# Performance work log

Measured on AMD Instinct MI355X. Metric: run time of the kernel, lower is better.

Reference implementation:

```python
import jax, jax.numpy as jnp
import numpy as np

N, H, DK, DV, DFF, D = 2, 8, 32, 32, 512, 256
B, S = 2, 2048
MASK_VALUE = -1e-30
EPS = 1e-14  # K.epsilon()**2 with default epsilon 1e-7


def glorot(key, shape):
    fan_in, fan_out = shape[-2], shape[-1]
    limit = np.sqrt(6.0 / (fan_in + fan_out))
    return jax.random.uniform(key, shape, jnp.float32, -limit, limit)


def setup_inputs() -> dict:
    key = jax.random.key(0)
    ks = jax.random.split(key, 8)
    return {
        "x": jax.random.normal(ks[0], (B, S, D), jnp.float32),
        "mask": jnp.ones((B, S), jnp.float32),
        "Wq": glorot(ks[1], (N, H, D, DK)),
        "Wk": glorot(ks[2], (N, H, D, DK)),
        "Wv": glorot(ks[3], (N, H, D, DV)),
        "Wo": glorot(ks[4], (N, H * DV, D)),
        "W1": glorot(ks[5], (N, D, DFF)),
        "b1": jnp.zeros((N, DFF), jnp.float32),
        "W2": glorot(ks[6], (N, DFF, D)),
        "b2": jnp.zeros((N, D), jnp.float32),
        "gamma": jnp.ones((2 * N,), jnp.float32),
        "beta": jnp.zeros((2 * N,), jnp.float32),
    }


def _layernorm(x, g, b):
    mean = jnp.mean(x, axis=-1, keepdims=True)
    var = jnp.mean(jnp.square(x - mean), axis=-1, keepdims=True)
    return (x - mean) / jnp.sqrt(var + EPS) * g + b


def reference(x, mask, Wq, Wk, Wv, Wo, W1, b1, W2, b2, gamma, beta):
    m = mask[:, None, None, :]  # [B,1,1,S], multiplies score rows' key axis
    for i in range(N):
        # batched multi-head attention (no 1/sqrt(dk) scaling, faithful to source)
        q = jnp.einsum("bsd,hdk->bhsk", x, Wq[i])
        k = jnp.einsum("bsd,hdk->bhsk", x, Wk[i])
        v = jnp.einsum("bsd,hdv->bhsv", x, Wv[i])
        A = jnp.einsum("bhsk,bhtk->bhst", q, k)  # [B,H,S,S]
        A = m * A + (1.0 - m) * MASK_VALUE
        A = jax.nn.softmax(A, axis=-1)
        o = jnp.einsum("bhst,bhtv->bhsv", A, v)
        conc = o.transpose(0, 2, 1, 3).reshape(x.shape[0], x.shape[1], H * DV)
        x = x + conc @ Wo[i]
        x = _layernorm(x, gamma[2 * i], beta[2 * i])
        ffn = jax.nn.relu(x @ W1[i] + b1[i]) @ W2[i] + b2[i]
        x = x + ffn
        x = _layernorm(x, gamma[2 * i + 1], beta[2 * i + 1])
    return x
```

## Files before the change

### kernel.cpp

```cpp
#include <hip/hip_runtime.h>
#include <hip/hip_bf16.h>

#define NL 2
#define NH 8
#define DKk 32
#define DVv 32
#define DFF 512
#define DD 256
#define BB 2
#define SS 2048
#define MROWS (BB*SS)
#define LN_EPS 1e-14f
#define L2E 1.4426950408889634f
#define SOFT_SHIFT_L2E (50.0f*L2E)

typedef __hip_bfloat16 bf16;
typedef unsigned short us;
typedef short bf16x8 __attribute__((ext_vector_type(8)));
typedef float f32x4  __attribute__((ext_vector_type(4)));
typedef unsigned short us4 __attribute__((ext_vector_type(4)));

#define O_XF   256
#define O_QB   (O_XF+1048576)
#define O_KH   (O_QB+1048576)
#define O_KL   (O_KH+524288)
#define O_VT   (O_KL+524288)
#define O_XH   (O_VT+524288)
#define O_XL   (O_XH+524288)
#define O_OP   (O_XL+524288)
#define O_ML   (O_OP+2097152)
#define O_MASK (O_ML+65536)
#define O_B1   (O_MASK+4096)
#define O_B2   (O_B1+1024)
#define O_GM   (O_B2+512)
#define O_BT   (O_GM+4)
#define O_PREP (O_BT+4)
#define TAIL_TOTAL (4096+1024+512+4+4)
#define CONV_BLOCKS (512 + (TAIL_TOTAL+255)/256)
#define PREP_BLOCKS 512
#define PQH 0u
#define PQL 393216u
#define POH 786432u
#define POL 917504u
#define P1H 1048576u
#define P1L 1310720u
#define P2H 1572864u
#define P2L 1835008u

__device__ __forceinline__ float us2f(us u){
  unsigned int v = ((unsigned int)u) << 16; float f;
  __builtin_memcpy(&f, &v, 4); return f;
}
__device__ __forceinline__ us f2bf_rne(float f){
  unsigned int b = __float_as_uint(f);
  b += 0x7FFFu + ((b>>16)&1u);
  return (us)(b>>16);
}

#if __has_builtin(__builtin_amdgcn_exp2f)
#define EXP2F(x) __builtin_amdgcn_exp2f(x)
#else
#define EXP2F(x) exp2f(x)
#endif

#if __has_builtin(__builtin_amdgcn_cvt_pk_bf16_f32)
typedef __bf16 bf16x2_t __attribute__((ext_vector_type(2)));
__device__ __forceinline__ int pack_bf16(float a, float b){
  bf16x2_t r = __builtin_amdgcn_cvt_pk_bf16_f32(a, b);
  int i; __builtin_memcpy(&i, &r, 4); return i;
}
#else
__device__ __forceinline__ int pack_bf16(float a, float b){
  int b0 = __float_as_int(a) + 0x8000;
  int b1 = __float_as_int(b) + 0x8000;
  return (b1 & 0xFFFF0000) | ((int)((unsigned)b0 >> 16));
}
#endif

__device__ __forceinline__ void gl_lds16(const us* g, us* l){
  __builtin_amdgcn_global_load_lds(
    (const __attribute__((address_space(1))) unsigned int*)g,
    (__attribute__((address_space(3))) unsigned int*)l, 16, 0, 0);
}

__device__ __forceinline__ size_t xhl_idx(int row, int col){
  int rt = row>>6, rg = (row>>4)&3, L15 = row&15;
  int kc = col>>5, Q = (col>>3)&3, j = col&7;
  return ((size_t)(rt*8+kc))*2048 + rg*512 + Q*128 + L15*8 + j;
}

__device__ __forceinline__ float conv1(const void* src, size_t i, int flag){
  if(flag) return ((const float*)src)[i];
  return us2f(((const us*)src)[i]);
}

__device__ __forceinline__ void prep_b_raw(const void* W0, const void* W1v, const void* W2v,
                                           int baseoff, us* __restrict__ Bh, us* __restrict__ Bl,
                                           int Kd, int Nd, int qkv, int g, int flag)
{
  int total = (Kd/32)*(Nd/16)*64;
  if(g >= total) return;
  int lane = g & 63, fi = g >> 6;
  int ncN = Nd/16;
  int nc = fi % ncN, kc = fi / ncN;
  int Q = lane>>4, L15 = lane&15;
  int n = nc*16 + L15;
  const void* src;
  int off0, stride;
  if(qkv){
    int sec = n>>8, h = (n>>5)&7, kq = n&31;
    src = (sec==0)?W0:((sec==1)?W1v:W2v);
    off0 = baseoff + h*8192 + kq;
    stride = 32;
  } else {
    src = W0;
    off0 = baseoff + n;
    stride = Nd;
  }
  #pragma unroll
  for(int j=0;j<8;j++){
    int k = kc*32 + Q*8 + j;
    float v = conv1(src, (size_t)off0 + (size_t)k*stride, flag);
    us hb = f2bf_rne(v);
    Bh[(size_t)g*8 + j] = hb;
    Bl[(size_t)g*8 + j] = f2bf_rne(v - us2f(hb));
  }
}

__global__ void conv_prep(const void* s0, const void* s1, const void* sWq, const void* sWk,
                          const void* sWv, const void* sWo, const void* sW1, const void* sb1,
                          const void* sW2, const void* sb2, const void* sgm, const void* sbt,
                          float* __restrict__ ws, int* __restrict__ flagp)
{
  __shared__ int fsh[4];
  int bad = 0;
  const us* xr = (const us*)s0;
  for(int i=threadIdx.x; i<4096; i+=256){
    float f = us2f(xr[i]);
    if(!(fabsf(f) < 1e3f)) bad = 1;
  }
  unsigned long long m = __ballot(bad);
  if((threadIdx.x&63)==0) fsh[threadIdx.x>>6] = (m!=0ull);
  __syncthreads();
  int flag = (fsh[0]|fsh[1]|fsh[2]|fsh[3]);
  if(blockIdx.x==0 && threadIdx.x==0) *flagp = flag;

  int b = blockIdx.x;
  if(b < PREP_BLOCKS){
    int layer = b >> 8, lb = b & 255;
    us* prep = (us*)(ws + O_PREP);
    if(lb < 96){
      int g = lb*256 + threadIdx.x;
      prep_b_raw(sWq, sWk, sWv, layer*65536, prep+PQH+(size_t)layer*196608,
                 prep+PQL+(size_t)layer*196608, 256, 768, 1, g, flag);
    } else if(lb < 128){
      int g = (lb-96)*256 + threadIdx.x;
      prep_b_raw(sWo, nullptr, nullptr, layer*65536, prep+POH+(size_t)layer*65536,
                 prep+POL+(size_t)layer*65536, 256, 256, 0, g, flag);
    } else if(lb < 192){
      int g = (lb-128)*256 + threadIdx.x;
      prep_b_raw(sW1, nullptr, nullptr, layer*131072, prep+P1H+(size_t)layer*131072,
                 prep+P1L+(size_t)layer*131072, 256, 512, 0, g, flag);
    } else {
      int g = (lb-192)*256 + threadIdx.x;
      prep_b_raw(sW2, nullptr, nullptr, layer*131072, prep+P2H+(size_t)layer*131072,
                 prep+P2L+(size_t)layer*131072, 512, 256, 0, g, flag);
    }
    return;
  }
  int b2 = b - PREP_BLOCKS;
  if(b2 < 512){
    int g8 = b2*256 + threadIdx.x;
    int e0 = g8*8;
    float v[8];
    if(flag){
      float4 a0 = *((const float4*)s0 + (e0>>2));
      float4 a1 = *((const float4*)s0 + (e0>>2) + 1);
      v[0]=a0.x; v[1]=a0.y; v[2]=a0.z; v[3]=a0.w;
      v[4]=a1.x; v[5]=a1.y; v[6]=a1.z; v[7]=a1.w;
    } else {
      bf16x8 u = *((const bf16x8*)s0 + g8);
      #pragma unroll
      for(int j=0;j<8;j++) v[j] = us2f((us)u[j]);
    }
    *(float4*)&ws[O_XF+e0]   = (float4){v[0],v[1],v[2],v[3]};
    *(float4*)&ws[O_XF+e0+4] = (float4){v[4],v[5],v[6],v[7]};
    union{ us a[8]; uint4 q; } hh, ll;
    #pragma unroll
    for(int j=0;j<8;j++){
      us hb = f2bf_rne(v[j]);
      hh.a[j] = hb;
      ll.a[j] = f2bf_rne(v[j] - us2f(hb));
    }
    size_t xi = xhl_idx(e0>>8, e0&255);
    *(uint4*)&((us*)(ws+O_XH))[xi] = hh.q;
    *(uint4*)&((us*)(ws+O_XL))[xi] = ll.q;
    return;
  }
  int g = (b2-512)*256 + threadIdx.x;
  if(g < 4096){ ws[O_MASK+g] = conv1(s1, g, flag)*L2E; return; }
  g -= 4096;
  if(g < 1024){ ws[O_B1+g] = conv1(sb1, g, flag); return; }
  g -= 1024;
  if(g < 512){ ws[O_B2+g] = conv1(sb2, g, flag); return; }
  g -= 512;
  if(g < 4){ ws[O_GM+g] = conv1(sgm, g, flag); return; }
  g -= 4;
  if(g < 4){ ws[O_BT+g] = conv1(sbt, g, flag); return; }
}

template<int MODE>
__launch_bounds__(256)
__global__ void gemm_mfma(const us* __restrict__ Axh, const us* __restrict__ Axl,
                          const us* __restrict__ Bh, const us* __restrict__ Bl,
                          const float* __restrict__ bias,
                          float* __restrict__ O,
                          us* __restrict__ QH, us* __restrict__ QL,
                          us* __restrict__ KH, us* __restrict__ KL, us* __restrict__ VT,
                          int Ncols, int Kdim)
{
  __shared__ __align__(16) us SH[16384];
  const int t = threadIdx.x;
  const int w = t>>6, lane = t&63;
  const int Q = lane>>4, L15 = lane&15;
  const int bx = blockIdx.x, by = blockIdx.y;
  const int row0 = bx*64;
  const int nc0 = by*4;
  const int col0 = by*64;
  const int nKc = Kdim>>5;
  const int ncW = Ncols>>4;

  f32x4 acc[2][2];
  #pragma unroll
  for(int i=0;i<2;i++)
    #pragma unroll
    for(int j=0;j<2;j++) acc[i][j] = (f32x4){0.f,0.f,0.f,0.f};

  auto stage = [&](int kc){
    const int bo = (kc&1)*8192;
    size_t abase = ((size_t)(bx*nKc + kc))*2048;
    gl_lds16(&Axh[abase + (size_t)t*8], &SH[bo + t*8]);
    gl_lds16(&Axl[abase + (size_t)t*8], &SH[bo + 2048 + t*8]);
    size_t gidx = ((size_t)(kc*ncW + nc0 + w)*64 + lane)*8;
    gl_lds16(&Bh[gidx], &SH[bo + 4096 + t*8]);
    gl_lds16(&Bl[gidx], &SH[bo + 6144 + t*8]);
  };

  stage(0);

  for(int kc=0; kc<nKc; kc++){
    __syncthreads();
    if(kc+1 < nKc) stage(kc+1);
    const int bo = (kc&1)*8192;
    const us* Ah  = SH + bo;
    const us* Al  = SH + bo + 2048;
    const us* Bhs = SH + bo + 4096;
    const us* Bls = SH + bo + 6144;

    bf16x8 aAh[2], aAl[2], bBh[2], bBl[2];
    #pragma unroll
    for(int rg2=0;rg2<2;rg2++){
      int rg = (w&1)*2 + rg2;
      aAh[rg2] = *(const bf16x8*)&Ah[rg*512 + lane*8];
      aAl[rg2] = *(const bf16x8*)&Al[rg*512 + lane*8];
    }
    #pragma unroll
    for(int cg2=0;cg2<2;cg2++){
      int nc = (w>>1)*2 + cg2;
      bBh[cg2] = *(const bf16x8*)&Bhs[nc*512 + lane*8];
      bBl[cg2] = *(const bf16x8*)&Bls[nc*512 + lane*8];
    }
    #pragma unroll
    for(int rg2=0;rg2<2;rg2++)
      #pragma unroll
      for(int cg2=0;cg2<2;cg2++){
        acc[rg2][cg2] = __builtin_amdgcn_mfma_f32_16x16x32_bf16(aAl[rg2], bBh[cg2], acc[rg2][cg2], 0,0,0);
        acc[rg2][cg2] = __builtin_amdgcn_mfma_f32_16x16x32_bf16(aAh[rg2], bBl[cg2], acc[rg2][cg2], 0,0,0);
        acc[rg2][cg2] = __builtin_amdgcn_mfma_f32_16x16x32_bf16(aAh[rg2], bBh[cg2], acc[rg2][cg2], 0,0,0);
      }
  }

  if(MODE==0){
    __syncthreads();
    us* TH = SH;
    us* TL = SH + 4608;
    #pragma unroll
    for(int rg2=0;rg2<2;rg2++)
      #pragma unroll
      for(int cg2=0;cg2<2;cg2++)
        #pragma unroll
        for(int r=0;r<4;r++){
          int rl = (w&1)*32 + rg2*16 + Q*4 + r;
          int cl = (w>>1)*32 + cg2*16 + L15;
          float va = acc[rg2][cg2][r];
          us hb = f2bf_rne(va);
          TH[rl*72+cl] = hb;
          TL[rl*72+cl] = f2bf_rne(va - us2f(hb));
        }
    __syncthreads();
    const int sec = col0>>8;
    const int h0  = (col0&255)>>5;
    const int b_  = row0>>11;
    const int srow0 = row0 & 2047;
    if(sec < 2){
      us* DH = (sec==0) ? QH : KH;
      us* DL = (sec==0) ? QL : KL;
      #pragma unroll
      for(int u2=0; u2<2; u2++){
        int u = w + u2*4;
        int rg = u&3, half = u>>2;
        int lbase = (rg*16 + L15)*72 + half*32 + Q*8;
        bf16x8 hv = *(const bf16x8*)&TH[lbase];
        bf16x8 lv = *(const bf16x8*)&TL[lbase];
        int bh = b_*NH + h0 + half;
        size_t dbase = ((size_t)(bh*128 + (srow0>>4) + rg)*64 + lane)*8;
        *(bf16x8*)&DH[dbase] = hv;
        *(bf16x8*)&DL[dbase] = lv;
      }
    } else {
      #pragma unroll
      for(int u2=0; u2<2; u2++){
        int u = w + u2*4;
        int sgrp = u&1, kqh = (u>>1)&1, half = u>>2;
        union{ us u8[8]; bf16x8 v; } vv;
        #pragma unroll
        for(int j=0;j<8;j++){
          int rl = sgrp*32 + Q*8 + j;
          int cl = half*32 + kqh*16 + L15;
          vv.u8[j] = TH[rl*72+cl];
        }
        int bh = b_*NH + h0 + half;
        size_t dbase = ((size_t)((bh*64 + (srow0>>5) + sgrp)*2 + kqh)*64 + lane)*8;
        *(bf16x8*)&VT[dbase] = vv.v;
      }
    }
  } else {
    #pragma unroll
    for(int rg2=0;rg2<2;rg2++)
      #pragma unroll
      for(int cg2=0;cg2<2;cg2++)
        #pragma unroll
        for(int r=0;r<4;r++){
          int row = row0 + (w&1)*32 + rg2*16 + Q*4 + r;
          int c   = col0 + (w>>1)*32 + cg2*16 + L15;
          float v = acc[rg2][cg2][r] + bias[c];
          O[(size_t)row*Ncols + c] = v>0.f ? v : 0.f;
        }
  }
}

template<int SRC>
__launch_bounds__(256)
__global__ void gemm_ln(const float* __restrict__ A,
                        const float* __restrict__ OpartA, const float* __restrict__ MLA,
                        const us* __restrict__ Bh, const us* __restrict__ Bl,
                        const float* __restrict__ bias, const float* __restrict__ res,
                        float* __restrict__ xf,
                        us* __restrict__ xh, us* __restrict__ xl,
                        const float* __restrict__ gamma, const float* __restrict__ beta, int gi,
                        void* __restrict__ out, int write_out,
                        const int* __restrict__ flagp, int Kdim)
{
  __shared__ __align__(16) us Ahs[1024], Als[1024];
  __shared__ __align__(16) us Bhs[16384], Bls[16384];
  __shared__ float lred[128];
  const int t = threadIdx.x;
  const int w = t>>6, lane = t&63;
  const int Q = lane>>4, L15 = lane&15;
  const int row0 = blockIdx.x*16;
  const int nKc = Kdim>>5;

  f32x4 acc[4];
  #pragma unroll
  for(int cg=0;cg<4;cg++) acc[cg] = (f32x4){0.f,0.f,0.f,0.f};

  float4 pv0, pv1, pv;
  float pl0 = 0.f, pl1 = 0.f;

  auto preloadA = [&](int kc){
    if(t < 128){
      int r = t>>3;
      int kl = (t&7)*4;
      if(SRC==0){
        int row = row0 + r;
        int b_ = row>>11, s_ = row&2047;
        size_t i0 = (size_t)(b_*8 + kc)*2048 + s_;
        pl0 = MLA[i0];
        pl1 = MLA[i0+32768];
        pv0 = *(const float4*)&OpartA[i0*32 + kl];
        pv1 = *(const float4*)&OpartA[(i0+32768)*32 + kl];
      } else {
        pv = *(const float4*)&A[(size_t)(row0+r)*Kdim + kc*32 + kl];
      }
    }
  };
  auto writeA = [&](int kc){
    if(t < 128){
      int r = t>>3;
      int kl = (t&7)*4;
      float f[4];
      if(SRC==0){
        float inv = 1.f/(pl0 + pl1);
        f[0]=(pv0.x+pv1.x)*inv; f[1]=(pv0.y+pv1.y)*inv;
        f[2]=(pv0.z+pv1.z)*inv; f[3]=(pv0.w+pv1.w)*inv;
      } else {
        f[0]=pv.x; f[1]=pv.y; f[2]=pv.z; f[3]=pv.w;
      }
      us4 h4, l4;
      #pragma unroll
      for(int j=0;j<4;j++){
        us hb = f2bf_rne(f[j]);
        h4[j] = hb; l4[j] = f2bf_rne(f[j] - us2f(hb));
      }
      int bo = (kc&1)*512;
      int off = (kl>>3)*128 + r*8 + (kl&7);
      *(us4*)&Ahs[bo+off] = h4;
      *(us4*)&Als[bo+off] = l4;
    }
  };
  auto stageB = [&](int kc){
    const int bo = (kc&1)*8192;
    #pragma unroll
    for(int ii=0; ii<4; ii++){
      int unit = w + ii*4;
      size_t gidx = ((size_t)(kc*16 + unit)*64 + lane)*8;
      gl_lds16(&Bh[gidx], &Bhs[bo + unit*512 + lane*8]);
      gl_lds16(&Bl[gidx], &Bls[bo + unit*512 + lane*8]);
    }
  };

  preloadA(0);
  stageB(0);
  writeA(0);

  for(int kc=0; kc<nKc; kc++){
    __syncthreads();
    if(kc+1 < nKc){
      preloadA(kc+1);
      stageB(kc+1);
    }
    const int bo = (kc&1);
    bf16x8 aAh = *(const bf16x8*)&Ahs[bo*512 + lane*8];
    bf16x8 aAl = *(const bf16x8*)&Als[bo*512 + lane*8];
    #pragma unroll
    for(int cg=0;cg<4;cg++){
      int unit = w*4 + cg;
      bf16x8 bBh = *(const bf16x8*)&Bhs[bo*8192 + unit*512 + lane*8];
      bf16x8 bBl = *(const bf16x8*)&Bls[bo*8192 + unit*512 + lane*8];
      acc[cg] = __builtin_amdgcn_mfma_f32_16x16x32_bf16(aAl, bBh, acc[cg], 0,0,0);
      acc[cg] = __builtin_amdgcn_mfma_f32_16x16x32_bf16(aAh, bBl, acc[cg], 0,0,0);
      acc[cg] = __builtin_amdgcn_mfma_f32_16x16x32_bf16(aAh, bBh, acc[cg], 0,0,0);
    }
    if(kc+1 < nKc) writeA(kc+1);
  }

  float tmp[4][4];
  #pragma unroll
  for(int cg=0;cg<4;cg++)
    #pragma unroll
    for(int r=0;r<4;r++){
      int row = row0 + Q*4 + r;
      int c = w*64 + cg*16 + L15;
      float v = acc[cg][r] + res[(size_t)row*DD + c];
      if(SRC==1) v += bias[c];
      tmp[cg][r] = v;
    }
  float s[4], sq[4];
  #pragma unroll
  for(int r=0;r<4;r++){
    s[r]  = tmp[0][r]+tmp[1][r]+tmp[2][r]+tmp[3][r];
    sq[r] = tmp[0][r]*tmp[0][r]+tmp[1][r]*tmp[1][r]+tmp[2][r]*tmp[2][r]+tmp[3][r]*tmp[3][r];
  }
  #pragma unroll
  for(int off=1; off<16; off<<=1)
    #pragma unroll
    for(int r=0;r<4;r++){
      s[r]  += __shfl_xor(s[r], off);
      sq[r] += __shfl_xor(sq[r], off);
    }
  if(L15==0){
    #pragma unroll
    for(int r=0;r<4;r++){
      int rl = Q*4 + r;
      lred[(w*16 + rl)*2]   = s[r];
      lred[(w*16 + rl)*2+1] = sq[r];
    }
  }
  __syncthreads();
  float g = gamma[gi], bb = beta[gi];
  float scv[4], mnv[4];
  #pragma unroll
  for(int r=0;r<4;r++){
    int rl = Q*4 + r;
    float S  = lred[rl*2]   + lred[(16+rl)*2]   + lred[(32+rl)*2]   + lred[(48+rl)*2];
    float SQ = lred[rl*2+1] + lred[(16+rl)*2+1] + lred[(32+rl)*2+1] + lred[(48+rl)*2+1];
    float mean = S*(1.f/DD);
    float var  = SQ*(1.f/DD) - mean*mean;
    scv[r] = rsqrtf(var+LN_EPS)*g;
    mnv[r] = mean;
  }
  int flag = write_out ? *flagp : 0;
  #pragma unroll
  for(int cg=0;cg<4;cg++)
    #pragma unroll
    for(int r=0;r<4;r++){
      int row = row0 + Q*4 + r;
      int c = w*64 + cg*16 + L15;
      float val = (tmp[cg][r]-mnv[r])*scv[r] + bb;
      xf[(size_t)row*DD + c] = val;
      us hb = f2bf_rne(val);
      size_t xi = xhl_idx(row, c);
      xh[xi] = hb;
      xl[xi] = f2bf_rne(val - us2f(hb));
      if(write_out){
        if(flag) ((float*)out)[(size_t)row*DD + c] = val;
        else     ((bf16*)out)[(size_t)row*DD + c] = __float2bfloat16(val);
      }
    }
}

__launch_bounds__(256)
__global__ void attn_kernel(const us* __restrict__ QH, const us* __restrict__ QL,
                            const us* __restrict__ KH, const us* __restrict__ KL,
                            const us* __restrict__ VT,
                            const float* __restrict__ mask,
                            float* __restrict__ Opart, float* __restrict__ ML)
{
  __shared__ __align__(16) us Khs[4096], Kls[4096], Vts[4096];
  __shared__ __align__(16) float Msl[1024];
  const int t = threadIdx.x;
  const int swz = (blockIdx.x & 7)*128 + (blockIdx.x >> 3);
  const int bh = swz >> 6;
  const int qt = (swz & 63) >> 1;
  const int ks = swz & 1;
  const int b_ = bh >> 3;
  const int wv = t >> 6;
  const int lane = t & 63;
  const int Q = lane >> 4, L15 = lane & 15;
  const int q0 = qt*64 + wv*16;

  size_t qidx = ((size_t)(bh*128 + qt*4 + wv)*64 + lane)*8;
  const bf16x8 qh_v = *(const bf16x8*)&QH[qidx];
  const bf16x8 ql_v = *(const bf16x8*)&QL[qidx];

  const us* KHbh = KH + (size_t)bh*65536;
  const us* KLbh = KL + (size_t)bh*65536;
  const us* VTbh = VT + (size_t)bh*65536;
  const int base = ks*1024;

  f32x4 Oa0a = {0.f,0.f,0.f,0.f}, Oa0b = {0.f,0.f,0.f,0.f};
  f32x4 Oa1a = {0.f,0.f,0.f,0.f}, Oa1b = {0.f,0.f,0.f,0.f};
  float lacc = 0.f;

  {
    const us* mrow = (const us*)(mask + (size_t)b_*SS + base);
    gl_lds16(mrow + (size_t)t*8, ((us*)Msl) + t*8);
    size_t kbase = (size_t)(base>>4)*512;
    size_t vbase = (size_t)(base>>5)*1024;
    gl_lds16(&KHbh[kbase + (size_t)t*8], &Khs[t*8]);
    gl_lds16(&KLbh[kbase + (size_t)t*8], &Kls[t*8]);
    gl_lds16(&VTbh[vbase + (size_t)t*8], &Vts[t*8]);
  }

  for(int s=0; s<16; s++){
    __syncthreads();
    if(s < 15){
      int t0n = base + (s+1)*64;
      int bn = (s+1)&1;
      size_t kbase = (size_t)(t0n>>4)*512;
      size_t vbase = (size_t)(t0n>>5)*1024;
      gl_lds16(&KHbh[kbase + (size_t)t*8], &Khs[bn*2048 + t*8]);
      gl_lds16(&KLbh[kbase + (size_t)t*8], &Kls[bn*2048 + t*8]);
      gl_lds16(&VTbh[vbase + (size_t)t*8], &Vts[bn*2048 + t*8]);
    }
    const int bo = (s&1)*2048;
    const int mo = s*64;

    f32x4 St[4];
    const f32x4 zz = {0.f,0.f,0.f,0.f};
    #pragma unroll
    for(int kt=0;kt<4;kt++){
      bf16x8 aKh = *(const bf16x8*)&Khs[bo + kt*512 + lane*8];
      bf16x8 aKl = *(const bf16x8*)&Kls[bo + kt*512 + lane*8];
      f32x4 a = __builtin_amdgcn_mfma_f32_16x16x32_bf16(aKl, qh_v, zz, 0,0,0);
      a = __builtin_amdgcn_mfma_f32_16x16x32_bf16(aKh, ql_v, a, 0,0,0);
      a = __builtin_amdgcn_mfma_f32_16x16x32_bf16(aKh, qh_v, a, 0,0,0);
      St[kt] = a;
    }

    float lsum = 0.f;
    #pragma unroll
    for(int kt=0;kt<4;kt++){
      float4 mv = *(const float4*)&Msl[mo + kt*16 + Q*4];
      float mvr[4] = {mv.x, mv.y, mv.z, mv.w};
      #pragma unroll
      for(int r=0;r<4;r++){
        float p = EXP2F(fmaf(mvr[r], St[kt][r], -SOFT_SHIFT_L2E));
        St[kt][r] = p;
        lsum += p;
      }
    }
    lacc += lsum;

    int pk[4][2];
    #pragma unroll
    for(int kt=0;kt<4;kt++){
      pk[kt][0] = pack_bf16(St[kt][0], St[kt][1]);
      pk[kt][1] = pack_bf16(St[kt][2], St[kt][3]);
    }

    #pragma unroll
    for(int c=0;c<2;c++){
      union { int i[4]; bf16x8 v; } bu;
      #pragma unroll
      for(int d=0;d<4;d++){
        int srcl = (((Q&1)*2 + (d>>1))<<4) | L15;
        int vlo = __shfl(pk[2*c  ][d&1], srcl, 64);
        int vhi = __shfl(pk[2*c+1][d&1], srcl, 64);
        bu.i[d] = (Q & 2) ? vhi : vlo;
      }
      bf16x8 aV0 = *(const bf16x8*)&Vts[bo + (c*2+0)*512 + lane*8];
      bf16x8 aV1 = *(const bf16x8*)&Vts[bo + (c*2+1)*512 + lane*8];
      if(c == 0){
        Oa0a = __builtin_amdgcn_mfma_f32_16x16x32_bf16(aV0, bu.v, Oa0a, 0,0,0);
        Oa1a = __builtin_amdgcn_mfma_f32_16x16x32_bf16(aV1, bu.v, Oa1a, 0,0,0);
      } else {
        Oa0b = __builtin_amdgcn_mfma_f32_16x16x32_bf16(aV0, bu.v, Oa0b, 0,0,0);
        Oa1b = __builtin_amdgcn_mfma_f32_16x16x32_bf16(aV1, bu.v, Oa1b, 0,0,0);
      }
    }
  }

  f32x4 Oa0 = Oa0a + Oa0b;
  f32x4 Oa1 = Oa1a + Oa1b;
  lacc += __shfl_xor(lacc, 16);
  lacc += __shfl_xor(lacc, 32);

  float* opp = &Opart[((size_t)(ks*16+bh)*SS + q0 + L15)*32];
  #pragma unroll
  for(int r=0;r<4;r++){
    opp[Q*4+r]    = Oa0[r];
    opp[16+Q*4+r] = Oa1[r];
  }
  if(Q==0){
    ML[(size_t)(ks*16+bh)*SS + q0 + L15] = lacc;
  }
}

extern "C" void kernel_launch(void* const* d_in, const int* in_sizes, int n_in,
                              void* d_out, int out_size, void* d_ws, size_t ws_size,
                              hipStream_t stream)
{
  float* ws = (float*)d_ws;
  int* flagp = (int*)d_ws;

  float* xf  = ws + O_XF;
  us* QHb = (us*)(ws + O_QB);
  us* QLb = QHb + 1048576;
  us* KH = (us*)(ws + O_KH);
  us* KL = (us*)(ws + O_KL);
  us* VT = (us*)(ws + O_VT);
  us* XH = (us*)(ws + O_XH);
  us* XL = (us*)(ws + O_XL);
  float* Opart = ws + O_OP;
  float* ML  = ws + O_ML;
  float* fh  = Opart;
  float* b1f = ws + O_B1;
  float* b2f_ = ws + O_B2;
  float* gmf = ws + O_GM;
  float* btf = ws + O_BT;
  us* prep = (us*)(ws + O_PREP);

  conv_prep<<<PREP_BLOCKS+CONV_BLOCKS,256,0,stream>>>(
      d_in[0], d_in[1], d_in[2], d_in[3], d_in[4], d_in[5],
      d_in[6], d_in[7], d_in[8], d_in[9], d_in[10], d_in[11],
      ws, flagp);

  for(int i=0;i<NL;i++){
    const float* b1i = b1f + (size_t)i*DFF;
    const float* b2i = b2f_ + (size_t)i*DD;

    dim3 g0(64, 12);
    gemm_mfma<0><<<g0,256,0,stream>>>(XH, XL,
                                      prep+PQH+(size_t)i*196608, prep+PQL+(size_t)i*196608,
                                      nullptr, nullptr,
                                      QHb, QLb, KH, KL, VT, 768, 256);
    attn_kernel<<<1024,256,0,stream>>>(QHb, QLb, KH, KL, VT, ws + O_MASK, Opart, ML);
    gemm_ln<0><<<256,256,0,stream>>>(nullptr, Opart, ML,
                                     prep+POH+(size_t)i*65536, prep+POL+(size_t)i*65536,
                                     nullptr, xf, xf, XH, XL,
                                     gmf, btf, 2*i, d_out, 0, flagp, 256);
    dim3 g2(64, 8);
    gemm_mfma<2><<<g2,256,0,stream>>>(XH, XL,
                                      prep+P1H+(size_t)i*131072, prep+P1L+(size_t)i*131072,
                                      b1i, fh,
                                      nullptr, nullptr, nullptr, nullptr, nullptr, 512, 256);
    gemm_ln<1><<<256,256,0,stream>>>(fh, nullptr, nullptr,
                                     prep+P2H+(size_t)i*131072, prep+P2L+(size_t)i*131072,
                                     b2i, xf, xf, XH, XL,
                                     gmf, btf, 2*i+1, d_out, (i==NL-1)?1:0, flagp, 512);
  }
}
```

Baseline: 265.5 us.

## Fuse FFN up-projection, ReLU, down-projection and layernorm into one kernel

```diff
diff --git a/kernel.cpp b/kernel.cpp
--- a/kernel.cpp
+++ b/kernel.cpp
@@ -520,6 +520,168 @@
 }
 
 __launch_bounds__(256)
+__global__ void ffn_ln(const us* __restrict__ XHg, const us* __restrict__ XLg,
+                       const us* __restrict__ W1h, const us* __restrict__ W1l,
+                       const us* __restrict__ W2h, const us* __restrict__ W2l,
+                       const float* __restrict__ b1, const float* __restrict__ b2,
+                       const float* __restrict__ res,
+                       float* __restrict__ xf, us* __restrict__ xh, us* __restrict__ xl,
+                       const float* __restrict__ gamma, const float* __restrict__ beta, int gi,
+                       void* __restrict__ out, int write_out, const int* __restrict__ flagp)
+{
+  __shared__ __align__(16) us SH[32768];
+  __shared__ __align__(16) us hAH[8192], hAL[8192];
+  __shared__ float lred[128];
+  const int t = threadIdx.x;
+  const int w = t>>6, lane = t&63;
+  const int Q = lane>>4, L15 = lane&15;
+  const int row0 = blockIdx.x*16;
+  const int rt = row0>>6, rg = (row0>>4)&3;
+
+  auto stageW = [&](const us* Bh, const us* Bl, int fi0, int buf){
+    const int bo = buf*16384;
+    #pragma unroll
+    for(int ii=0; ii<4; ii++){
+      int u = w + ii*4;
+      size_t gidx = ((size_t)(fi0 + u)*64 + lane)*8;
+      gl_lds16(&Bh[gidx], &SH[bo + u*512 + lane*8]);
+      gl_lds16(&Bl[gidx], &SH[bo + 8192 + u*512 + lane*8]);
+    }
+  };
+
+  f32x4 acc_y[4];
+  #pragma unroll
+  for(int cg=0;cg<4;cg++) acc_y[cg] = (f32x4){0.f,0.f,0.f,0.f};
+
+  stageW(W1h, W1l, 0, 0);
+
+  int step = 0;
+  for(int nch=0; nch<2; nch++){
+    f32x4 acc_h[4];
+    #pragma unroll
+    for(int cg=0;cg<4;cg++) acc_h[cg] = (f32x4){0.f,0.f,0.f,0.f};
+    for(int kc=0; kc<8; kc++){
+      __syncthreads();
+      int ns = step + 1;
+      if(ns < 16){
+        int nnch = ns>>3, nkc = ns&7;
+        stageW(W1h, W1l, nkc*32 + nnch*16, ns&1);
+      } else {
+        stageW(W2h, W2l, 0, ns&1);
+      }
+      const int bo = (step&1)*16384;
+      size_t abase = ((size_t)(rt*8+kc))*2048 + (size_t)rg*512 + (size_t)lane*8;
+      bf16x8 aAh = *(const bf16x8*)&XHg[abase];
+      bf16x8 aAl = *(const bf16x8*)&XLg[abase];
+      #pragma unroll
+      for(int cg=0;cg<4;cg++){
+        int u = w*4 + cg;
+        bf16x8 bBh = *(const bf16x8*)&SH[bo + u*512 + lane*8];
+        bf16x8 bBl = *(const bf16x8*)&SH[bo + 8192 + u*512 + lane*8];
+        acc_h[cg] = __builtin_amdgcn_mfma_f32_16x16x32_bf16(aAl, bBh, acc_h[cg], 0,0,0);
+        acc_h[cg] = __builtin_amdgcn_mfma_f32_16x16x32_bf16(aAh, bBl, acc_h[cg], 0,0,0);
+        acc_h[cg] = __builtin_amdgcn_mfma_f32_16x16x32_bf16(aAh, bBh, acc_h[cg], 0,0,0);
+      }
+      step++;
+    }
+    #pragma unroll
+    for(int cg=0;cg<4;cg++){
+      int col = nch*256 + (w*4+cg)*16 + L15;
+      float bv = b1[col];
+      int base = (col>>5)*512 + (((col&31)>>3))*128 + (col&7);
+      #pragma unroll
+      for(int r=0;r<4;r++){
+        int row = Q*4 + r;
+        float v = acc_h[cg][r] + bv;
+        v = v>0.f ? v : 0.f;
+        us hb = f2bf_rne(v);
+        hAH[base + row*8] = hb;
+        hAL[base + row*8] = f2bf_rne(v - us2f(hb));
+      }
+    }
+  }
+  for(int kc2=0; kc2<16; kc2++){
+    __syncthreads();
+    if(kc2+1 < 16) stageW(W2h, W2l, (kc2+1)*16, (step+1)&1);
+    const int bo = (step&1)*16384;
+    bf16x8 aAh = *(const bf16x8*)&hAH[kc2*512 + lane*8];
+    bf16x8 aAl = *(const bf16x8*)&hAL[kc2*512 + lane*8];
+    #pragma unroll
+    for(int cg=0;cg<4;cg++){
+      int u = w*4 + cg;
+      bf16x8 bBh = *(const bf16x8*)&SH[bo + u*512 + lane*8];
+      bf16x8 bBl = *(const bf16x8*)&SH[bo + 8192 + u*512 + lane*8];
+      acc_y[cg] = __builtin_amdgcn_mfma_f32_16x16x32_bf16(aAl, bBh, acc_y[cg], 0,0,0);
+      acc_y[cg] = __builtin_amdgcn_mfma_f32_16x16x32_bf16(aAh, bBl, acc_y[cg], 0,0,0);
+      acc_y[cg] = __builtin_amdgcn_mfma_f32_16x16x32_bf16(aAh, bBh, acc_y[cg], 0,0,0);
+    }
+    step++;
+  }
+
+  float tmp[4][4];
+  #pragma unroll
+  for(int cg=0;cg<4;cg++)
+    #pragma unroll
+    for(int r=0;r<4;r++){
+      int row = row0 + Q*4 + r;
+      int c = w*64 + cg*16 + L15;
+      tmp[cg][r] = acc_y[cg][r] + res[(size_t)row*DD + c] + b2[c];
+    }
+  float s[4], sq[4];
+  #pragma unroll
+  for(int r=0;r<4;r++){
+    s[r]  = tmp[0][r]+tmp[1][r]+tmp[2][r]+tmp[3][r];
+    sq[r] = tmp[0][r]*tmp[0][r]+tmp[1][r]*tmp[1][r]+tmp[2][r]*tmp[2][r]+tmp[3][r]*tmp[3][r];
+  }
+  #pragma unroll
+  for(int off=1; off<16; off<<=1)
+    #pragma unroll
+    for(int r=0;r<4;r++){
+      s[r]  += __shfl_xor(s[r], off);
+      sq[r] += __shfl_xor(sq[r], off);
+    }
+  if(L15==0){
+    #pragma unroll
+    for(int r=0;r<4;r++){
+      int rl = Q*4 + r;
+      lred[(w*16 + rl)*2]   = s[r];
+      lred[(w*16 + rl)*2+1] = sq[r];
+    }
+  }
+  __syncthreads();
+  float g = gamma[gi], bb = beta[gi];
+  float scv[4], mnv[4];
+  #pragma unroll
+  for(int r=0;r<4;r++){
+    int rl = Q*4 + r;
+    float S  = lred[rl*2]   + lred[(16+rl)*2]   + lred[(32+rl)*2]   + lred[(48+rl)*2];
+    float SQ = lred[rl*2+1] + lred[(16+rl)*2+1] + lred[(32+rl)*2+1] + lred[(48+rl)*2+1];
+    float mean = S*(1.f/DD);
+    float var  = SQ*(1.f/DD) - mean*mean;
+    scv[r] = rsqrtf(var+LN_EPS)*g;
+    mnv[r] = mean;
+  }
+  int flag = write_out ? *flagp : 0;
+  #pragma unroll
+  for(int cg=0;cg<4;cg++)
+    #pragma unroll
+    for(int r=0;r<4;r++){
+      int row = row0 + Q*4 + r;
+      int c = w*64 + cg*16 + L15;
+      float val = (tmp[cg][r]-mnv[r])*scv[r] + bb;
+      xf[(size_t)row*DD + c] = val;
+      us hb = f2bf_rne(val);
+      size_t xi = xhl_idx(row, c);
+      xh[xi] = hb;
+      xl[xi] = f2bf_rne(val - us2f(hb));
+      if(write_out){
+        if(flag) ((float*)out)[(size_t)row*DD + c] = val;
+        else     ((bf16*)out)[(size_t)row*DD + c] = __float2bfloat16(val);
+      }
+    }
+}
+
+__launch_bounds__(256)
 __global__ void attn_kernel(const us* __restrict__ QH, const us* __restrict__ QL,
                             const us* __restrict__ KH, const us* __restrict__ KL,
                             const us* __restrict__ VT,
@@ -529,10 +691,9 @@
   __shared__ __align__(16) us Khs[4096], Kls[4096], Vts[4096];
   __shared__ __align__(16) float Msl[1024];
   const int t = threadIdx.x;
-  const int swz = (blockIdx.x & 7)*128 + (blockIdx.x >> 3);
-  const int bh = swz >> 6;
-  const int qt = (swz & 63) >> 1;
-  const int ks = swz & 1;
+  const int bh = blockIdx.x >> 6;
+  const int qt = (blockIdx.x & 63) >> 1;
+  const int ks = blockIdx.x & 1;
   const int b_ = bh >> 3;
   const int wv = t >> 6;
   const int lane = t & 63;
@@ -664,7 +825,6 @@
   us* XL = (us*)(ws + O_XL);
   float* Opart = ws + O_OP;
   float* ML  = ws + O_ML;
-  float* fh  = Opart;
   float* b1f = ws + O_B1;
   float* b2f_ = ws + O_B2;
   float* gmf = ws + O_GM;
@@ -690,14 +850,10 @@
                                      prep+POH+(size_t)i*65536, prep+POL+(size_t)i*65536,
                                      nullptr, xf, xf, XH, XL,
                                      gmf, btf, 2*i, d_out, 0, flagp, 256);
-    dim3 g2(64, 8);
-    gemm_mfma<2><<<g2,256,0,stream>>>(XH, XL,
-                                      prep+P1H+(size_t)i*131072, prep+P1L+(size_t)i*131072,
-                                      b1i, fh,
-                                      nullptr, nullptr, nullptr, nullptr, nullptr, 512, 256);
-    gemm_ln<1><<<256,256,0,stream>>>(fh, nullptr, nullptr,
-                                     prep+P2H+(size_t)i*131072, prep+P2L+(size_t)i*131072,
-                                     b2i, xf, xf, XH, XL,
-                                     gmf, btf, 2*i+1, d_out, (i==NL-1)?1:0, flagp, 512);
-  }
-}
+    ffn_ln<<<256,256,0,stream>>>(XH, XL,
+                                 prep+P1H+(size_t)i*131072, prep+P1L+(size_t)i*131072,
+                                 prep+P2H+(size_t)i*131072, prep+P2L+(size_t)i*131072,
+                                 b1i, b2i, xf, xf, XH, XL,
+                                 gmf, btf, 2*i+1, d_out, (i==NL-1)?1:0, flagp);
+  }
+}
```

Result: no change. 261.6 us (-1.5%).
